# Optimization experiments

Measured on AMD Instinct MI355X. Metric: run time of the kernel, lower is better.

## Reference

```python
import jax, jax.numpy as jnp
import numpy as np

B, T, D, H = 4, 4096, 1024, 64

def setup_inputs() -> dict:
    key = jax.random.key(0)
    k1, k2, k3, k4 = jax.random.split(key, 4)
    scale = 1.0 / np.sqrt(D)
    return {
        "x": jax.random.normal(k1, (B, T, D), dtype=jnp.float32),
        "Wq": jax.random.normal(k2, (D, H), dtype=jnp.float32) * scale,
        "Wk": jax.random.normal(k3, (D, H), dtype=jnp.float32) * scale,
        "Wv": jax.random.normal(k4, (D, H), dtype=jnp.float32) * scale,
    }

def reference(x, Wq, Wk, Wv):
    # Projections (Linear without bias): [B,T,H]
    q = jnp.einsum('btd,dh->bth', x, Wq)
    k = jnp.einsum('btd,dh->bth', x, Wk)
    v = jnp.einsum('btd,dh->bth', x, Wv)
    head_size = q.shape[-1]
    # Full T x T scores, scaled by sqrt(head_size) as in the source
    attn = jnp.einsum('bqh,bkh->bqk', q, k) / jnp.sqrt(jnp.float32(head_size))
    t = x.shape[1]
    causal = jnp.tril(jnp.ones((t, t), dtype=bool))  # [T,T]
    attn = jnp.where(causal[None, :, :], attn, -jnp.inf)
    attn = jax.nn.softmax(attn, axis=-1)
    # dropout prob = 0.0 -> identity
    out = jnp.einsum('bqk,bkh->bqh', attn, v)
    return out
```

## Files before the change

### kernel.cpp

```cpp
#include <hip/hip_runtime.h>
#include <hip/hip_bf16.h>
#include <math.h>

#define BB 4
#define TT 4096
#define DD 1024
#define HH 64
#define MTOT (BB * TT)
#define NCH 4

typedef short short8 __attribute__((ext_vector_type(8)));
typedef float f32x4  __attribute__((ext_vector_type(4)));
typedef unsigned int u32;

__device__ __forceinline__ unsigned short f2bf(float f) {
    unsigned u = __builtin_bit_cast(unsigned, f);
    unsigned r = (u + 0x7fffu + ((u >> 16) & 1u)) >> 16;
    return (unsigned short)r;
}

__device__ __forceinline__ unsigned long long pack4(float a, float b, float c, float d) {
    return (unsigned long long)f2bf(a) |
           ((unsigned long long)f2bf(b) << 16) |
           ((unsigned long long)f2bf(c) << 32) |
           ((unsigned long long)f2bf(d) << 48);
}

__device__ __forceinline__ short8 pack8(float4 a, float4 b) {
    short8 r;
    r[0] = (short)f2bf(a.x); r[1] = (short)f2bf(a.y);
    r[2] = (short)f2bf(a.z); r[3] = (short)f2bf(a.w);
    r[4] = (short)f2bf(b.x); r[5] = (short)f2bf(b.y);
    r[6] = (short)f2bf(b.z); r[7] = (short)f2bf(b.w);
    return r;
}

__device__ __forceinline__ void gl16(const void* g, void* l) {
    __builtin_amdgcn_global_load_lds(
        (const __attribute__((address_space(1))) u32*)g,
        (__attribute__((address_space(3))) u32*)l, 16, 0, 0);
}

#define QOFF  0
#define KOFF  (MTOT * HH)
#define VOFF  (2 * MTOT * HH)
#define BF_TOTAL (3 * MTOT * HH)

__global__ __launch_bounds__(256) void transpose_w(
    const float* __restrict__ Wq, const float* __restrict__ Wk,
    const float* __restrict__ Wv, unsigned short* __restrict__ Wt)
{
    const int w = blockIdx.y;
    const float* W = (w == 0) ? Wq : (w == 1) ? Wk : Wv;
    unsigned short* o = Wt + (size_t)w * 64 * 1024;
    const int t  = threadIdx.x;
    const int n4 = t & 15;
    const int k0 = blockIdx.x * 64 + (t >> 4) * 4;

    float v[4][4];
#pragma unroll
    for (int ii = 0; ii < 4; ++ii) {
        float4 r = *(const float4*)&W[(size_t)(k0 + ii) * HH + n4 * 4];
        v[ii][0] = r.x; v[ii][1] = r.y; v[ii][2] = r.z; v[ii][3] = r.w;
    }
#pragma unroll
    for (int cc = 0; cc < 4; ++cc) {
        unsigned long long pk = pack4(v[0][cc], v[1][cc], v[2][cc], v[3][cc]);
        *(unsigned long long*)&o[(size_t)(n4 * 4 + cc) * 1024 + k0] = pk;
    }
}

__global__ __launch_bounds__(256, 2) void qkv_proj(
    const float* __restrict__ x,
    const unsigned short* __restrict__ Wt,
    unsigned short* __restrict__ qkv)
{
    const int tid   = threadIdx.x;
    const int lane  = tid & 63;
    const int wave  = tid >> 6;
    const int l15   = lane & 15;
    const int quad  = lane >> 4;
    const int m0    = blockIdx.x * 32;
    const int strip = wave & 1;
    const int half  = wave >> 1;

    __shared__ float          Af[2][32 * 64];
    __shared__ unsigned short Bs[2][192 * 64];

    const int ar  = lane >> 4;
    const int as  = lane & 15;
    const int bc  = lane >> 3;
    const int bs2 = (lane & 7) ^ bc;

#define STAGEW(it, p)                                                        \
    {                                                                        \
        const int kc_ = (it) * 64;                                           \
        _Pragma("unroll")                                                    \
        for (int jj = 0; jj < 2; ++jj) {                                     \
            int j   = wave * 2 + jj;                                         \
            int row = 4 * j + ar;                                            \
            int sw  = as ^ (row & 15);                                       \
            gl16(x + (size_t)(m0 + row) * DD + kc_ + sw * 4,                 \
                 &Af[p][j * 256]);                                           \
        }                                                                    \
        _Pragma("unroll")                                                    \
        for (int jj = 0; jj < 6; ++jj) {                                     \
            int j    = wave * 6 + jj;                                        \
            int gcol = 8 * j + bc;                                           \
            gl16(Wt + (size_t)gcol * 1024 + kc_ + bs2 * 8,                   \
                 &Bs[p][j * 512]);                                           \
        }                                                                    \
    }

    f32x4 acc[6];
#pragma unroll
    for (int i = 0; i < 6; ++i) acc[i] = (f32x4){0.f, 0.f, 0.f, 0.f};

    STAGEW(0, 0)
    __syncthreads();
    int p = 0;

    for (int it = 0; it < 16; ++it) {
        if (it < 15) STAGEW(it + 1, p ^ 1)

        const int row = strip * 16 + l15;
#pragma unroll
        for (int ks = 0; ks < 2; ++ks) {
            int c0 = ks * 8 + quad * 2;
            float4 a0 = *(const float4*)&Af[p][row * 64 + ((c0)     ^ l15) * 4];
            float4 a1 = *(const float4*)&Af[p][row * 64 + ((c0 + 1) ^ l15) * 4];
            short8 af = pack8(a0, a1);
            int cb = (ks * 4 + quad) ^ (l15 & 7);
#pragma unroll
            for (int jj = 0; jj < 6; ++jj) {
                int col = (half * 6 + jj) * 16 + l15;
                short8 bfr = *(const short8*)&Bs[p][col * 64 + cb * 8];
                acc[jj] = __builtin_amdgcn_mfma_f32_16x16x32_bf16(af, bfr, acc[jj], 0, 0, 0);
            }
        }
        __syncthreads();
        p ^= 1;
    }
#undef STAGEW

    const float QS = 0.125f * 1.44269504088896f;
    unsigned short* q_bf  = qkv + QOFF;
    unsigned short* k_bf  = qkv + KOFF;
    unsigned short* vt_bf = qkv + VOFF;
#pragma unroll
    for (int jj = 0; jj < 6; ++jj) {
        int g = half * 6 + jj, w = g >> 2, col = (g & 3) * 16 + l15;
#pragma unroll
        for (int r = 0; r < 4; ++r) {
            int m = m0 + strip * 16 + quad * 4 + r;
            float val = acc[jj][r];
            if (w == 0) val *= QS;
            unsigned short bv = f2bf(val);
            if (w == 0)      q_bf[(size_t)m * HH + col] = bv;
            else if (w == 1) k_bf[(size_t)m * HH + col] = bv;
            else {
                int b = m >> 12, t = m & 4095;
                vt_bf[(size_t)b * HH * TT + (size_t)col * TT + t] = bv;
            }
        }
    }
}

__global__ __launch_bounds__(256) void flash_attn(
    const unsigned short* __restrict__ qkv,
    float* __restrict__ Opart,
    float* __restrict__ Mpart,
    float* __restrict__ Lpart)
{
    const int qt = 63 - blockIdx.x;
    const int b  = blockIdx.y;
    const int c  = blockIdx.z;
    if (c * 16 > qt) return;
    const int j0   = c * 16;
    const int jmax = min(j0 + 16, qt + 1);

    const int tid  = threadIdx.x;
    const int lane = tid & 63;
    const int wave = tid >> 6;
    const int l15  = lane & 15;
    const int quad = lane >> 4;

    const unsigned short* q_g  = qkv + QOFF + (size_t)b * TT * HH;
    const unsigned short* k_g  = qkv + KOFF + (size_t)b * TT * HH;
    const unsigned short* vt_g = qkv + VOFF + (size_t)b * HH * TT;

    __shared__ unsigned short Ks[2][128 * 64];
    __shared__ unsigned short Vs[2][64 * 128];
    __shared__ unsigned short Ps[4][16 * 72];
    unsigned short* Pw = &Ps[wave][0];

    const int kr3 = lane >> 3;
    const int kch = lane & 7;
    const int vr2 = lane >> 4;
    const int vch = lane & 15;

#define STAGE(jr_, p_)                                                        \
    {                                                                         \
        const unsigned short* kp = k_g  + (size_t)(jr_) * 64 * HH;            \
        const unsigned short* vp = vt_g + (size_t)(jr_) * 64;                 \
        _Pragma("unroll")                                                     \
        for (int i = 0; i < 4; ++i) {                                         \
            int g = wave * 4 + i;                                             \
            gl16(kp + (size_t)(g * 8 + kr3) * HH + (kch ^ kr3) * 8,           \
                 &Ks[p_][g * 512]);                                           \
        }                                                                     \
        _Pragma("unroll")                                                     \
        for (int i = 0; i < 4; ++i) {                                         \
            int g = wave * 4 + i;                                             \
            int h = g * 4 + vr2;                                              \
            gl16(vp + (size_t)h * TT + (vch ^ (h & 15)) * 8,                  \
                 &Vs[p_][g * 512]);                                           \
        }                                                                     \
    }

    short8 qf[2];
#pragma unroll
    for (int kk = 0; kk < 2; ++kk)
        qf[kk] = *(const short8*)&q_g[(size_t)(qt * 64 + wave * 16 + l15) * HH + kk * 32 + quad * 8];

    f32x4 ov[4];
#pragma unroll
    for (int i = 0; i < 4; ++i) ov[i] = (f32x4){0.f, 0.f, 0.f, 0.f};
    float m_run = -1e30f, l_run = 0.f;

    STAGE(j0, 0)
    __syncthreads();
    int p = 0;

    for (int jr = j0; jr < jmax; jr += 2) {
        const bool two = (jmax - jr) >= 2;

        if (jr + 2 < jmax) STAGE(jr + 2, p ^ 1)

        f32x4 st0[4], st1[4];
#pragma unroll
        for (int i = 0; i < 4; ++i) {
            st0[i] = (f32x4){0.f, 0.f, 0.f, 0.f};
            st1[i] = (f32x4){0.f, 0.f, 0.f, 0.f};
        }
#pragma unroll
        for (int kk = 0; kk < 2; ++kk)
#pragma unroll
            for (int mt = 0; mt < 4; ++mt) {
                short8 a = *(const short8*)&Ks[p][(mt * 16 + l15) * 64 +
                                                  (((kk * 4 + quad) ^ (l15 & 7)) * 8)];
                st0[mt] = __builtin_amdgcn_mfma_f32_16x16x32_bf16(a, qf[kk], st0[mt], 0, 0, 0);
            }
        if (two) {
#pragma unroll
            for (int kk = 0; kk < 2; ++kk)
#pragma unroll
                for (int mt = 0; mt < 4; ++mt) {
                    short8 a = *(const short8*)&Ks[p][(64 + mt * 16 + l15) * 64 +
                                                      (((kk * 4 + quad) ^ (l15 & 7)) * 8)];
                    st1[mt] = __builtin_amdgcn_mfma_f32_16x16x32_bf16(a, qf[kk], st1[mt], 0, 0, 0);
                }
        }

        const int qg = wave * 16 + l15;
        if (jr == qt) {
#pragma unroll
            for (int mt = 0; mt < 4; ++mt)
#pragma unroll
                for (int r = 0; r < 4; ++r)
                    if (mt * 16 + quad * 4 + r > qg) st0[mt][r] = -1e30f;
        } else if (two && jr + 1 == qt) {
#pragma unroll
            for (int mt = 0; mt < 4; ++mt)
#pragma unroll
                for (int r = 0; r < 4; ++r)
                    if (mt * 16 + quad * 4 + r > qg) st1[mt][r] = -1e30f;
        }

        float mloc = -1e30f;
#pragma unroll
        for (int mt = 0; mt < 4; ++mt)
#pragma unroll
            for (int r = 0; r < 4; ++r) mloc = fmaxf(mloc, st0[mt][r]);
        if (two) {
#pragma unroll
            for (int mt = 0; mt < 4; ++mt)
#pragma unroll
                for (int r = 0; r < 4; ++r) mloc = fmaxf(mloc, st1[mt][r]);
        }
        mloc = fmaxf(mloc, __shfl_xor(mloc, 16));
        mloc = fmaxf(mloc, __shfl_xor(mloc, 32));
        const float m_new = fmaxf(m_run, mloc);
        const float alpha = exp2f(m_run - m_new);
        m_run = m_new;

        float ssum = 0.f;
#pragma unroll
        for (int mt = 0; mt < 4; ++mt)
#pragma unroll
            for (int r = 0; r < 4; ++r) {
                float pv = exp2f(st0[mt][r] - m_new);
                st0[mt][r] = pv; ssum += pv;
            }
        if (two) {
#pragma unroll
            for (int mt = 0; mt < 4; ++mt)
#pragma unroll
                for (int r = 0; r < 4; ++r) {
                    float pv = exp2f(st1[mt][r] - m_new);
                    st1[mt][r] = pv; ssum += pv;
                }
        }
        ssum += __shfl_xor(ssum, 16);
        ssum += __shfl_xor(ssum, 32);
        l_run = l_run * alpha + ssum;

        {
            float a0 = __shfl(alpha, quad * 4 + 0);
            float a1 = __shfl(alpha, quad * 4 + 1);
            float a2 = __shfl(alpha, quad * 4 + 2);
            float a3 = __shfl(alpha, quad * 4 + 3);
#pragma unroll
            for (int ht = 0; ht < 4; ++ht) {
                ov[ht][0] *= a0; ov[ht][1] *= a1;
                ov[ht][2] *= a2; ov[ht][3] *= a3;
            }
        }

#pragma unroll
        for (int mt = 0; mt < 4; ++mt) {
            u32 p0, p1;
            asm("v_cvt_pk_bf16_f32 %0, %1, %2" : "=v"(p0) : "v"(st0[mt][0]), "v"(st0[mt][1]));
            asm("v_cvt_pk_bf16_f32 %0, %1, %2" : "=v"(p1) : "v"(st0[mt][2]), "v"(st0[mt][3]));
            uint2 pr; pr.x = p0; pr.y = p1;
            *(uint2*)&Pw[l15 * 72 + mt * 16 + quad * 4] = pr;
        }
#pragma unroll
        for (int kk = 0; kk < 2; ++kk) {
            short8 a = *(const short8*)&Pw[l15 * 72 + kk * 32 + quad * 8];
#pragma unroll
            for (int ht = 0; ht < 4; ++ht) {
                short8 bf = *(const short8*)&Vs[p][(ht * 16 + l15) * 128 +
                                                   (((kk * 4 + quad) ^ l15) * 8)];
                ov[ht] = __builtin_amdgcn_mfma_f32_16x16x32_bf16(a, bf, ov[ht], 0, 0, 0);
            }
        }

        if (two) {
#pragma unroll
            for (int mt = 0; mt < 4; ++mt) {
                u32 p0, p1;
                asm("v_cvt_pk_bf16_f32 %0, %1, %2" : "=v"(p0) : "v"(st1[mt][0]), "v"(st1[mt][1]));
                asm("v_cvt_pk_bf16_f32 %0, %1, %2" : "=v"(p1) : "v"(st1[mt][2]), "v"(st1[mt][3]));
                uint2 pr; pr.x = p0; pr.y = p1;
                *(uint2*)&Pw[l15 * 72 + mt * 16 + quad * 4] = pr;
            }
#pragma unroll
            for (int kk = 0; kk < 2; ++kk) {
                short8 a = *(const short8*)&Pw[l15 * 72 + kk * 32 + quad * 8];
#pragma unroll
                for (int ht = 0; ht < 4; ++ht) {
                    short8 bf = *(const short8*)&Vs[p][(ht * 16 + l15) * 128 +
                                                       (((8 + kk * 4 + quad) ^ l15) * 8)];
                    ov[ht] = __builtin_amdgcn_mfma_f32_16x16x32_bf16(a, bf, ov[ht], 0, 0, 0);
                }
            }
        }

        __syncthreads();
        p ^= 1;
    }
#undef STAGE

    float* Ob = Opart + ((size_t)((b * 64 + qt) * NCH + c)) * 4096;
#pragma unroll
    for (int ht = 0; ht < 4; ++ht)
#pragma unroll
        for (int r = 0; r < 4; ++r)
            Ob[(size_t)(wave * 16 + quad * 4 + r) * HH + ht * 16 + l15] = ov[ht][r];
    if (quad == 0) {
        size_t mi = (size_t)((b * 64 + qt) * NCH + c) * 64 + wave * 16 + l15;
        Mpart[mi] = m_run;
        Lpart[mi] = l_run;
    }
}

__global__ __launch_bounds__(256) void combine(
    const float* __restrict__ Opart,
    const float* __restrict__ Mpart,
    const float* __restrict__ Lpart,
    float* __restrict__ out)
{
    const int qt = blockIdx.x;
    const int b  = blockIdx.y;
    const int nc = (qt >> 4) + 1;
    const int t  = threadIdx.x;
    const int row = t >> 2;
    const int seg = t & 3;

    const size_t base = (size_t)(b * 64 + qt) * NCH;

    float m_c[NCH], M = -1e30f;
    for (int c = 0; c < nc; ++c) {
        m_c[c] = Mpart[(base + c) * 64 + row];
        M = fmaxf(M, m_c[c]);
    }
    float L = 0.f, w_c[NCH];
    for (int c = 0; c < nc; ++c) {
        w_c[c] = exp2f(m_c[c] - M);
        L += w_c[c] * Lpart[(base + c) * 64 + row];
    }
    float invL = 1.0f / L;

    f32x4 o[4];
#pragma unroll
    for (int i = 0; i < 4; ++i) o[i] = (f32x4){0.f, 0.f, 0.f, 0.f};
    for (int c = 0; c < nc; ++c) {
        const float* Ob = Opart + (base + c) * 4096 + (size_t)row * HH + seg * 16;
#pragma unroll
        for (int i = 0; i < 4; ++i) {
            f32x4 v = *(const f32x4*)(Ob + i * 4);
            o[i] += v * w_c[c];
        }
    }
    float* op = out + ((size_t)b * TT + qt * 64 + row) * HH + seg * 16;
#pragma unroll
    for (int i = 0; i < 4; ++i)
        *(f32x4*)(op + i * 4) = o[i] * invL;
}

extern "C" void kernel_launch(void* const* d_in, const int* in_sizes, int n_in,
                              void* d_out, int out_size, void* d_ws, size_t ws_size,
                              hipStream_t stream) {
    const float* x  = (const float*)d_in[0];
    const float* Wq = (const float*)d_in[1];
    const float* Wk = (const float*)d_in[2];
    const float* Wv = (const float*)d_in[3];
    float* out = (float*)d_out;

    unsigned short* qkv = (unsigned short*)d_ws;
    float* Opart = (float*)((char*)d_ws + BF_TOTAL * 2);
    float* Mpart = Opart + (size_t)BB * 64 * NCH * 4096;
    float* Lpart = Mpart + (size_t)BB * 64 * NCH * 64;

    unsigned short* Wt = (unsigned short*)d_out;

    transpose_w<<<dim3(16, 3), 256, 0, stream>>>(Wq, Wk, Wv, Wt);
    qkv_proj<<<dim3(MTOT / 32), 256, 0, stream>>>(x, Wt, qkv);
    flash_attn<<<dim3(64, BB, NCH), 256, 0, stream>>>(qkv, Opart, Mpart, Lpart);
    combine<<<dim3(64, BB), 256, 0, stream>>>(Opart, Mpart, Lpart, out);
}
```

Measured before the change: 163.0 us.

## Keep P in registers, single-buffer V with re-swizzled layout, raise occupancy

Softmax probabilities are packed to bf16 in registers and fed straight to the PV MFMA, removing the per-wave LDS round trip through Ps. V is now single-buffered and loaded inside the same iteration, with a new swizzle and split 8-byte reads that line up with the register layout of P. An extra barrier is added before the PV step. Launch bounds ask for 3 blocks per CU, using the LDS freed by dropping Ps and one V buffer. The cost is that V loads are no longer prefetched an iteration ahead, so their latency sits on the critical path, and the extra barrier adds a sync point.

Measured after the change: 154.9 us. 1.05x faster.

```diff
diff --git a/kernel.cpp b/kernel.cpp
--- a/kernel.cpp
+++ b/kernel.cpp
@@ -12,6 +12,7 @@
 typedef short short8 __attribute__((ext_vector_type(8)));
 typedef float f32x4  __attribute__((ext_vector_type(4)));
 typedef unsigned int u32;
+typedef unsigned long long u64;
 
 __device__ __forceinline__ unsigned short f2bf(float f) {
     unsigned u = __builtin_bit_cast(unsigned, f);
@@ -166,7 +167,7 @@
     }
 }
 
-__global__ __launch_bounds__(256) void flash_attn(
+__global__ __launch_bounds__(256, 3) void flash_attn(
     const unsigned short* __restrict__ qkv,
     float* __restrict__ Opart,
     float* __restrict__ Mpart,
@@ -190,31 +191,32 @@
     const unsigned short* vt_g = qkv + VOFF + (size_t)b * HH * TT;
 
     __shared__ unsigned short Ks[2][128 * 64];
-    __shared__ unsigned short Vs[2][64 * 128];
-    __shared__ unsigned short Ps[4][16 * 72];
-    unsigned short* Pw = &Ps[wave][0];
+    __shared__ unsigned short Vs[64 * 128];
 
     const int kr3 = lane >> 3;
     const int kch = lane & 7;
     const int vr2 = lane >> 4;
     const int vch = lane & 15;
 
-#define STAGE(jr_, p_)                                                        \
+#define STAGE_K(jr_, p_)                                                      \
     {                                                                         \
-        const unsigned short* kp = k_g  + (size_t)(jr_) * 64 * HH;            \
-        const unsigned short* vp = vt_g + (size_t)(jr_) * 64;                 \
+        const unsigned short* kp = k_g + (size_t)(jr_) * 64 * HH;             \
         _Pragma("unroll")                                                     \
         for (int i = 0; i < 4; ++i) {                                         \
             int g = wave * 4 + i;                                             \
             gl16(kp + (size_t)(g * 8 + kr3) * HH + (kch ^ kr3) * 8,           \
                  &Ks[p_][g * 512]);                                           \
         }                                                                     \
+    }
+#define STAGE_V(jr_)                                                          \
+    {                                                                         \
+        const unsigned short* vp = vt_g + (size_t)(jr_) * 64;                 \
         _Pragma("unroll")                                                     \
         for (int i = 0; i < 4; ++i) {                                         \
             int g = wave * 4 + i;                                             \
             int h = g * 4 + vr2;                                              \
-            gl16(vp + (size_t)h * TT + (vch ^ (h & 15)) * 8,                  \
-                 &Vs[p_][g * 512]);                                           \
+            gl16(vp + (size_t)h * TT + (vch ^ ((h >> 1) & 7)) * 8,            \
+                 &Vs[g * 512]);                                               \
         }                                                                     \
     }
 
@@ -228,14 +230,17 @@
     for (int i = 0; i < 4; ++i) ov[i] = (f32x4){0.f, 0.f, 0.f, 0.f};
     float m_run = -1e30f, l_run = 0.f;
 
-    STAGE(j0, 0)
+    STAGE_K(j0, 0)
     __syncthreads();
     int p = 0;
 
+    const int swv = 2 * ((l15 >> 1) & 7);
+
     for (int jr = j0; jr < jmax; jr += 2) {
         const bool two = (jmax - jr) >= 2;
 
-        if (jr + 2 < jmax) STAGE(jr + 2, p ^ 1)
+        STAGE_V(jr)
+        if (jr + 2 < jmax) STAGE_K(jr + 2, p ^ 1)
 
         f32x4 st0[4], st1[4];
 #pragma unroll
@@ -315,6 +320,32 @@
         ssum += __shfl_xor(ssum, 32);
         l_run = l_run * alpha + ssum;
 
+        short8 pa00, pa01, pa10, pa11;
+        {
+            u32* pp = (u32*)&pa00;
+            asm("v_cvt_pk_bf16_f32 %0, %1, %2" : "=v"(pp[0]) : "v"(st0[0][0]), "v"(st0[0][1]));
+            asm("v_cvt_pk_bf16_f32 %0, %1, %2" : "=v"(pp[1]) : "v"(st0[0][2]), "v"(st0[0][3]));
+            asm("v_cvt_pk_bf16_f32 %0, %1, %2" : "=v"(pp[2]) : "v"(st0[1][0]), "v"(st0[1][1]));
+            asm("v_cvt_pk_bf16_f32 %0, %1, %2" : "=v"(pp[3]) : "v"(st0[1][2]), "v"(st0[1][3]));
+            pp = (u32*)&pa01;
+            asm("v_cvt_pk_bf16_f32 %0, %1, %2" : "=v"(pp[0]) : "v"(st0[2][0]), "v"(st0[2][1]));
+            asm("v_cvt_pk_bf16_f32 %0, %1, %2" : "=v"(pp[1]) : "v"(st0[2][2]), "v"(st0[2][3]));
+            asm("v_cvt_pk_bf16_f32 %0, %1, %2" : "=v"(pp[2]) : "v"(st0[3][0]), "v"(st0[3][1]));
+            asm("v_cvt_pk_bf16_f32 %0, %1, %2" : "=v"(pp[3]) : "v"(st0[3][2]), "v"(st0[3][3]));
+        }
+        if (two) {
+            u32* pp = (u32*)&pa10;
+            asm("v_cvt_pk_bf16_f32 %0, %1, %2" : "=v"(pp[0]) : "v"(st1[0][0]), "v"(st1[0][1]));
+            asm("v_cvt_pk_bf16_f32 %0, %1, %2" : "=v"(pp[1]) : "v"(st1[0][2]), "v"(st1[0][3]));
+            asm("v_cvt_pk_bf16_f32 %0, %1, %2" : "=v"(pp[2]) : "v"(st1[1][0]), "v"(st1[1][1]));
+            asm("v_cvt_pk_bf16_f32 %0, %1, %2" : "=v"(pp[3]) : "v"(st1[1][2]), "v"(st1[1][3]));
+            pp = (u32*)&pa11;
+            asm("v_cvt_pk_bf16_f32 %0, %1, %2" : "=v"(pp[0]) : "v"(st1[2][0]), "v"(st1[2][1]));
+            asm("v_cvt_pk_bf16_f32 %0, %1, %2" : "=v"(pp[1]) : "v"(st1[2][2]), "v"(st1[2][3]));
+            asm("v_cvt_pk_bf16_f32 %0, %1, %2" : "=v"(pp[2]) : "v"(st1[3][0]), "v"(st1[3][1]));
+            asm("v_cvt_pk_bf16_f32 %0, %1, %2" : "=v"(pp[3]) : "v"(st1[3][2]), "v"(st1[3][3]));
+        }
+
         {
             float a0 = __shfl(alpha, quad * 4 + 0);
             float a1 = __shfl(alpha, quad * 4 + 1);
@@ -327,42 +358,37 @@
             }
         }
 
-#pragma unroll
-        for (int mt = 0; mt < 4; ++mt) {
-            u32 p0, p1;
-            asm("v_cvt_pk_bf16_f32 %0, %1, %2" : "=v"(p0) : "v"(st0[mt][0]), "v"(st0[mt][1]));
-            asm("v_cvt_pk_bf16_f32 %0, %1, %2" : "=v"(p1) : "v"(st0[mt][2]), "v"(st0[mt][3]));
-            uint2 pr; pr.x = p0; pr.y = p1;
-            *(uint2*)&Pw[l15 * 72 + mt * 16 + quad * 4] = pr;
-        }
+        __syncthreads();
+
 #pragma unroll
         for (int kk = 0; kk < 2; ++kk) {
-            short8 a = *(const short8*)&Pw[l15 * 72 + kk * 32 + quad * 8];
+            short8 a = kk ? pa01 : pa00;
+            int c8 = kk * 8 + quad;
 #pragma unroll
             for (int ht = 0; ht < 4; ++ht) {
-                short8 bf = *(const short8*)&Vs[p][(ht * 16 + l15) * 128 +
-                                                   (((kk * 4 + quad) ^ l15) * 8)];
-                ov[ht] = __builtin_amdgcn_mfma_f32_16x16x32_bf16(a, bf, ov[ht], 0, 0, 0);
-            }
-        }
-
+                int rb = (ht * 16 + l15) * 128;
+                u64 lo = *(const u64*)&Vs[rb + ((c8 ^ swv) << 2)];
+                u64 hi = *(const u64*)&Vs[rb + ((c8 ^ 4 ^ swv) << 2)];
+                short8 vb;
+                ((u64*)&vb)[0] = lo;
+                ((u64*)&vb)[1] = hi;
+                ov[ht] = __builtin_amdgcn_mfma_f32_16x16x32_bf16(a, vb, ov[ht], 0, 0, 0);
+            }
+        }
         if (two) {
 #pragma unroll
-            for (int mt = 0; mt < 4; ++mt) {
-                u32 p0, p1;
-                asm("v_cvt_pk_bf16_f32 %0, %1, %2" : "=v"(p0) : "v"(st1[mt][0]), "v"(st1[mt][1]));
-                asm("v_cvt_pk_bf16_f32 %0, %1, %2" : "=v"(p1) : "v"(st1[mt][2]), "v"(st1[mt][3]));
-                uint2 pr; pr.x = p0; pr.y = p1;
-                *(uint2*)&Pw[l15 * 72 + mt * 16 + quad * 4] = pr;
-            }
-#pragma unroll
             for (int kk = 0; kk < 2; ++kk) {
-                short8 a = *(const short8*)&Pw[l15 * 72 + kk * 32 + quad * 8];
+                short8 a = kk ? pa11 : pa10;
+                int c8 = 16 + kk * 8 + quad;
 #pragma unroll
                 for (int ht = 0; ht < 4; ++ht) {
-                    short8 bf = *(const short8*)&Vs[p][(ht * 16 + l15) * 128 +
-                                                       (((8 + kk * 4 + quad) ^ l15) * 8)];
-                    ov[ht] = __builtin_amdgcn_mfma_f32_16x16x32_bf16(a, bf, ov[ht], 0, 0, 0);
+                    int rb = (ht * 16 + l15) * 128;
+                    u64 lo = *(const u64*)&Vs[rb + ((c8 ^ swv) << 2)];
+                    u64 hi = *(const u64*)&Vs[rb + ((c8 ^ 4 ^ swv) << 2)];
+                    short8 vb;
+                    ((u64*)&vb)[0] = lo;
+                    ((u64*)&vb)[1] = hi;
+                    ov[ht] = __builtin_amdgcn_mfma_f32_16x16x32_bf16(a, vb, ov[ht], 0, 0, 0);
                 }
             }
         }
@@ -370,7 +396,8 @@
         __syncthreads();
         p ^= 1;
     }
-#undef STAGE
+#undef STAGE_K
+#undef STAGE_V
 
     float* Ob = Opart + ((size_t)((b * 64 + qt) * NCH + c)) * 4096;
 #pragma unroll
```

## Process paired query tiles per block sharing K/V tiles, with finer KV chunking

Applied to the files above, without the earlier changes.

Each flash-attention block now handles two adjacent query tiles, so each K/V tile staged into shared memory is reused by both. KV work is split into 8 chunks of 8 tiles instead of 4 of 16, and blocks are mapped through a flattened 1D grid. P is kept in registers instead of going through shared memory, and V reads use a new swizzle. The rescale is skipped when the max does not change, s_setprio wraps the MFMA sections, and the bf16 packing in the projection kernel uses v_cvt_pk_bf16_f32. The change aims to cut LDS traffic per query and improve load balance, at the cost of more registers per thread (launch bounds 256,2) and more partial results for the combine step.

Result: slower. 181.8 us (+11.5%).

```diff
diff --git a/kernel.cpp b/kernel.cpp
--- a/kernel.cpp
+++ b/kernel.cpp
@@ -7,11 +7,12 @@
 #define DD 1024
 #define HH 64
 #define MTOT (BB * TT)
-#define NCH 4
+#define NCH 8
 
 typedef short short8 __attribute__((ext_vector_type(8)));
 typedef float f32x4  __attribute__((ext_vector_type(4)));
 typedef unsigned int u32;
+typedef unsigned long long u64;
 
 __device__ __forceinline__ unsigned short f2bf(float f) {
     unsigned u = __builtin_bit_cast(unsigned, f);
@@ -24,15 +25,6 @@
            ((unsigned long long)f2bf(b) << 16) |
            ((unsigned long long)f2bf(c) << 32) |
            ((unsigned long long)f2bf(d) << 48);
-}
-
-__device__ __forceinline__ short8 pack8(float4 a, float4 b) {
-    short8 r;
-    r[0] = (short)f2bf(a.x); r[1] = (short)f2bf(a.y);
-    r[2] = (short)f2bf(a.z); r[3] = (short)f2bf(a.w);
-    r[4] = (short)f2bf(b.x); r[5] = (short)f2bf(b.y);
-    r[6] = (short)f2bf(b.z); r[7] = (short)f2bf(b.w);
-    return r;
 }
 
 __device__ __forceinline__ void gl16(const void* g, void* l) {
@@ -129,7 +121,14 @@
             int c0 = ks * 8 + quad * 2;
             float4 a0 = *(const float4*)&Af[p][row * 64 + ((c0)     ^ l15) * 4];
             float4 a1 = *(const float4*)&Af[p][row * 64 + ((c0 + 1) ^ l15) * 4];
-            short8 af = pack8(a0, a1);
+            short8 af;
+            {
+                u32* ap = (u32*)&af;
+                asm("v_cvt_pk_bf16_f32 %0, %1, %2" : "=v"(ap[0]) : "v"(a0.x), "v"(a0.y));
+                asm("v_cvt_pk_bf16_f32 %0, %1, %2" : "=v"(ap[1]) : "v"(a0.z), "v"(a0.w));
+                asm("v_cvt_pk_bf16_f32 %0, %1, %2" : "=v"(ap[2]) : "v"(a1.x), "v"(a1.y));
+                asm("v_cvt_pk_bf16_f32 %0, %1, %2" : "=v"(ap[3]) : "v"(a1.z), "v"(a1.w));
+            }
             int cb = (ks * 4 + quad) ^ (l15 & 7);
 #pragma unroll
             for (int jj = 0; jj < 6; ++jj) {
@@ -166,18 +165,22 @@
     }
 }
 
-__global__ __launch_bounds__(256) void flash_attn(
+__global__ __launch_bounds__(256, 2) void flash_attn(
     const unsigned short* __restrict__ qkv,
     float* __restrict__ Opart,
     float* __restrict__ Mpart,
     float* __restrict__ Lpart)
 {
-    const int qt = 63 - blockIdx.x;
-    const int b  = blockIdx.y;
-    const int c  = blockIdx.z;
-    if (c * 16 > qt) return;
-    const int j0   = c * 16;
-    const int jmax = min(j0 + 16, qt + 1);
+    const int gid = blockIdx.x;
+    const int b   = gid & 3;
+    const int u   = gid >> 2;
+    const int c   = u & 7;
+    const int pr  = u >> 3;
+    const int qtB = 63 - 2 * pr;
+    const int qtA = qtB - 1;
+    if (c * 8 > qtB) return;
+    const int j0   = c * 8;
+    const int jmax = min(j0 + 8, qtB + 1);
 
     const int tid  = threadIdx.x;
     const int lane = tid & 63;
@@ -189,199 +192,222 @@
     const unsigned short* k_g  = qkv + KOFF + (size_t)b * TT * HH;
     const unsigned short* vt_g = qkv + VOFF + (size_t)b * HH * TT;
 
-    __shared__ unsigned short Ks[2][128 * 64];
-    __shared__ unsigned short Vs[2][64 * 128];
-    __shared__ unsigned short Ps[4][16 * 72];
-    unsigned short* Pw = &Ps[wave][0];
-
-    const int kr3 = lane >> 3;
-    const int kch = lane & 7;
-    const int vr2 = lane >> 4;
-    const int vch = lane & 15;
-
-#define STAGE(jr_, p_)                                                        \
+    __shared__ unsigned short Ks[2][64 * 64];
+    __shared__ unsigned short Vs[2][64 * 64];
+
+    const int lr8 = lane >> 3;
+    const int lc8 = lane & 7;
+
+#define STAGE(j_, p_)                                                         \
     {                                                                         \
-        const unsigned short* kp = k_g  + (size_t)(jr_) * 64 * HH;            \
-        const unsigned short* vp = vt_g + (size_t)(jr_) * 64;                 \
+        const unsigned short* kp = k_g + (size_t)(j_) * 64 * HH;              \
+        const unsigned short* vp = vt_g + (size_t)(j_) * 64;                  \
         _Pragma("unroll")                                                     \
-        for (int i = 0; i < 4; ++i) {                                         \
-            int g = wave * 4 + i;                                             \
-            gl16(kp + (size_t)(g * 8 + kr3) * HH + (kch ^ kr3) * 8,           \
+        for (int i = 0; i < 2; ++i) {                                         \
+            int g = wave * 2 + i;                                             \
+            gl16(kp + (size_t)(g * 8 + lr8) * HH + ((lc8 ^ lr8) << 3),        \
                  &Ks[p_][g * 512]);                                           \
         }                                                                     \
         _Pragma("unroll")                                                     \
-        for (int i = 0; i < 4; ++i) {                                         \
-            int g = wave * 4 + i;                                             \
-            int h = g * 4 + vr2;                                              \
-            gl16(vp + (size_t)h * TT + (vch ^ (h & 15)) * 8,                  \
+        for (int i = 0; i < 2; ++i) {                                         \
+            int g = wave * 2 + i;                                             \
+            int sw = ((g & 1) << 2) | (lr8 >> 1);                             \
+            gl16(vp + (size_t)(g * 8 + lr8) * TT + ((lc8 ^ sw) << 3),         \
                  &Vs[p_][g * 512]);                                           \
         }                                                                     \
     }
 
-    short8 qf[2];
-#pragma unroll
-    for (int kk = 0; kk < 2; ++kk)
-        qf[kk] = *(const short8*)&q_g[(size_t)(qt * 64 + wave * 16 + l15) * HH + kk * 32 + quad * 8];
-
-    f32x4 ov[4];
-#pragma unroll
-    for (int i = 0; i < 4; ++i) ov[i] = (f32x4){0.f, 0.f, 0.f, 0.f};
-    float m_run = -1e30f, l_run = 0.f;
+    short8 qfA[2], qfB[2];
+#pragma unroll
+    for (int kk = 0; kk < 2; ++kk) {
+        qfA[kk] = *(const short8*)&q_g[(size_t)(qtA * 64 + wave * 16 + l15) * HH + kk * 32 + quad * 8];
+        qfB[kk] = *(const short8*)&q_g[(size_t)(qtB * 64 + wave * 16 + l15) * HH + kk * 32 + quad * 8];
+    }
+
+    f32x4 ovA[4], ovB[4];
+#pragma unroll
+    for (int i = 0; i < 4; ++i) {
+        ovA[i] = (f32x4){0.f, 0.f, 0.f, 0.f};
+        ovB[i] = (f32x4){0.f, 0.f, 0.f, 0.f};
+    }
+    float mA = -1e30f, lA = 0.f, mB = -1e30f, lB = 0.f;
 
     STAGE(j0, 0)
     __syncthreads();
     int p = 0;
 
-    for (int jr = j0; jr < jmax; jr += 2) {
-        const bool two = (jmax - jr) >= 2;
-
-        if (jr + 2 < jmax) STAGE(jr + 2, p ^ 1)
-
-        f32x4 st0[4], st1[4];
+    const int qg  = wave * 16 + l15;
+    const int swv = (l15 >> 1) & 7;
+
+    for (int j = j0; j < jmax; ++j) {
+        if (j + 1 < jmax) STAGE(j + 1, p ^ 1)
+        const bool doA = (j <= qtA);
+
+        f32x4 sA[4], sB[4];
 #pragma unroll
         for (int i = 0; i < 4; ++i) {
-            st0[i] = (f32x4){0.f, 0.f, 0.f, 0.f};
-            st1[i] = (f32x4){0.f, 0.f, 0.f, 0.f};
-        }
+            sA[i] = (f32x4){0.f, 0.f, 0.f, 0.f};
+            sB[i] = (f32x4){0.f, 0.f, 0.f, 0.f};
+        }
+        __builtin_amdgcn_s_setprio(1);
 #pragma unroll
         for (int kk = 0; kk < 2; ++kk)
 #pragma unroll
             for (int mt = 0; mt < 4; ++mt) {
                 short8 a = *(const short8*)&Ks[p][(mt * 16 + l15) * 64 +
-                                                  (((kk * 4 + quad) ^ (l15 & 7)) * 8)];
-                st0[mt] = __builtin_amdgcn_mfma_f32_16x16x32_bf16(a, qf[kk], st0[mt], 0, 0, 0);
-            }
-        if (two) {
-#pragma unroll
-            for (int kk = 0; kk < 2; ++kk)
-#pragma unroll
-                for (int mt = 0; mt < 4; ++mt) {
-                    short8 a = *(const short8*)&Ks[p][(64 + mt * 16 + l15) * 64 +
-                                                      (((kk * 4 + quad) ^ (l15 & 7)) * 8)];
-                    st1[mt] = __builtin_amdgcn_mfma_f32_16x16x32_bf16(a, qf[kk], st1[mt], 0, 0, 0);
+                                                  (((kk * 4 + quad) ^ (l15 & 7)) << 3)];
+                if (doA) sA[mt] = __builtin_amdgcn_mfma_f32_16x16x32_bf16(a, qfA[kk], sA[mt], 0, 0, 0);
+                sB[mt] = __builtin_amdgcn_mfma_f32_16x16x32_bf16(a, qfB[kk], sB[mt], 0, 0, 0);
+            }
+        __builtin_amdgcn_s_setprio(0);
+
+        short8 paA0 = {0}, paA1 = {0}, paB0 = {0}, paB1 = {0};
+        if (doA) {
+            if (j == qtA) {
+#pragma unroll
+                for (int mt = 0; mt < 4; ++mt)
+#pragma unroll
+                    for (int r = 0; r < 4; ++r)
+                        if (mt * 16 + quad * 4 + r > qg) sA[mt][r] = -1e30f;
+            }
+            float ml = -1e30f;
+#pragma unroll
+            for (int mt = 0; mt < 4; ++mt)
+#pragma unroll
+                for (int r = 0; r < 4; ++r) ml = fmaxf(ml, sA[mt][r]);
+            ml = fmaxf(ml, __shfl_xor(ml, 16));
+            ml = fmaxf(ml, __shfl_xor(ml, 32));
+            if (!__all(ml <= mA)) {
+                float mn = fmaxf(mA, ml);
+                float al = exp2f(mA - mn);
+                mA = mn;
+                lA *= al;
+                float a0 = __shfl(al, quad * 4 + 0);
+                float a1 = __shfl(al, quad * 4 + 1);
+                float a2 = __shfl(al, quad * 4 + 2);
+                float a3 = __shfl(al, quad * 4 + 3);
+#pragma unroll
+                for (int ht = 0; ht < 4; ++ht) {
+                    ovA[ht][0] *= a0; ovA[ht][1] *= a1;
+                    ovA[ht][2] *= a2; ovA[ht][3] *= a3;
                 }
-        }
-
-        const int qg = wave * 16 + l15;
-        if (jr == qt) {
+            }
+            float ss = 0.f;
 #pragma unroll
             for (int mt = 0; mt < 4; ++mt)
 #pragma unroll
-                for (int r = 0; r < 4; ++r)
-                    if (mt * 16 + quad * 4 + r > qg) st0[mt][r] = -1e30f;
-        } else if (two && jr + 1 == qt) {
+                for (int r = 0; r < 4; ++r) {
+                    float pv = exp2f(sA[mt][r] - mA);
+                    sA[mt][r] = pv; ss += pv;
+                }
+            ss += __shfl_xor(ss, 16);
+            ss += __shfl_xor(ss, 32);
+            lA += ss;
+            u32* pp = (u32*)&paA0;
+            asm("v_cvt_pk_bf16_f32 %0, %1, %2" : "=v"(pp[0]) : "v"(sA[0][0]), "v"(sA[0][1]));
+            asm("v_cvt_pk_bf16_f32 %0, %1, %2" : "=v"(pp[1]) : "v"(sA[0][2]), "v"(sA[0][3]));
+            asm("v_cvt_pk_bf16_f32 %0, %1, %2" : "=v"(pp[2]) : "v"(sA[1][0]), "v"(sA[1][1]));
+            asm("v_cvt_pk_bf16_f32 %0, %1, %2" : "=v"(pp[3]) : "v"(sA[1][2]), "v"(sA[1][3]));
+            pp = (u32*)&paA1;
+            asm("v_cvt_pk_bf16_f32 %0, %1, %2" : "=v"(pp[0]) : "v"(sA[2][0]), "v"(sA[2][1]));
+            asm("v_cvt_pk_bf16_f32 %0, %1, %2" : "=v"(pp[1]) : "v"(sA[2][2]), "v"(sA[2][3]));
+            asm("v_cvt_pk_bf16_f32 %0, %1, %2" : "=v"(pp[2]) : "v"(sA[3][0]), "v"(sA[3][1]));
+            asm("v_cvt_pk_bf16_f32 %0, %1, %2" : "=v"(pp[3]) : "v"(sA[3][2]), "v"(sA[3][3]));
+        }
+
+        {
+            if (j == qtB) {
+#pragma unroll
+                for (int mt = 0; mt < 4; ++mt)
+#pragma unroll
+                    for (int r = 0; r < 4; ++r)
+                        if (mt * 16 + quad * 4 + r > qg) sB[mt][r] = -1e30f;
+            }
+            float ml = -1e30f;
 #pragma unroll
             for (int mt = 0; mt < 4; ++mt)
 #pragma unroll
-                for (int r = 0; r < 4; ++r)
-                    if (mt * 16 + quad * 4 + r > qg) st1[mt][r] = -1e30f;
-        }
-
-        float mloc = -1e30f;
-#pragma unroll
-        for (int mt = 0; mt < 4; ++mt)
-#pragma unroll
-            for (int r = 0; r < 4; ++r) mloc = fmaxf(mloc, st0[mt][r]);
-        if (two) {
+                for (int r = 0; r < 4; ++r) ml = fmaxf(ml, sB[mt][r]);
+            ml = fmaxf(ml, __shfl_xor(ml, 16));
+            ml = fmaxf(ml, __shfl_xor(ml, 32));
+            if (!__all(ml <= mB)) {
+                float mn = fmaxf(mB, ml);
+                float al = exp2f(mB - mn);
+                mB = mn;
+                lB *= al;
+                float a0 = __shfl(al, quad * 4 + 0);
+                float a1 = __shfl(al, quad * 4 + 1);
+                float a2 = __shfl(al, quad * 4 + 2);
+                float a3 = __shfl(al, quad * 4 + 3);
+#pragma unroll
+                for (int ht = 0; ht < 4; ++ht) {
+                    ovB[ht][0] *= a0; ovB[ht][1] *= a1;
+                    ovB[ht][2] *= a2; ovB[ht][3] *= a3;
+                }
+            }
+            float ss = 0.f;
 #pragma unroll
             for (int mt = 0; mt < 4; ++mt)
 #pragma unroll
-                for (int r = 0; r < 4; ++r) mloc = fmaxf(mloc, st1[mt][r]);
-        }
-        mloc = fmaxf(mloc, __shfl_xor(mloc, 16));
-        mloc = fmaxf(mloc, __shfl_xor(mloc, 32));
-        const float m_new = fmaxf(m_run, mloc);
-        const float alpha = exp2f(m_run - m_new);
-        m_run = m_new;
-
-        float ssum = 0.f;
-#pragma unroll
-        for (int mt = 0; mt < 4; ++mt)
-#pragma unroll
-            for (int r = 0; r < 4; ++r) {
-                float pv = exp2f(st0[mt][r] - m_new);
-                st0[mt][r] = pv; ssum += pv;
-            }
-        if (two) {
-#pragma unroll
-            for (int mt = 0; mt < 4; ++mt)
-#pragma unroll
                 for (int r = 0; r < 4; ++r) {
-                    float pv = exp2f(st1[mt][r] - m_new);
-                    st1[mt][r] = pv; ssum += pv;
+                    float pv = exp2f(sB[mt][r] - mB);
+                    sB[mt][r] = pv; ss += pv;
                 }
-        }
-        ssum += __shfl_xor(ssum, 16);
-        ssum += __shfl_xor(ssum, 32);
-        l_run = l_run * alpha + ssum;
-
-        {
-            float a0 = __shfl(alpha, quad * 4 + 0);
-            float a1 = __shfl(alpha, quad * 4 + 1);
-            float a2 = __shfl(alpha, quad * 4 + 2);
-            float a3 = __shfl(alpha, quad * 4 + 3);
+            ss += __shfl_xor(ss, 16);
+            ss += __shfl_xor(ss, 32);
+            lB += ss;
+            u32* pp = (u32*)&paB0;
+            asm("v_cvt_pk_bf16_f32 %0, %1, %2" : "=v"(pp[0]) : "v"(sB[0][0]), "v"(sB[0][1]));
+            asm("v_cvt_pk_bf16_f32 %0, %1, %2" : "=v"(pp[1]) : "v"(sB[0][2]), "v"(sB[0][3]));
+            asm("v_cvt_pk_bf16_f32 %0, %1, %2" : "=v"(pp[2]) : "v"(sB[1][0]), "v"(sB[1][1]));
+            asm("v_cvt_pk_bf16_f32 %0, %1, %2" : "=v"(pp[3]) : "v"(sB[1][2]), "v"(sB[1][3]));
+            pp = (u32*)&paB1;
+            asm("v_cvt_pk_bf16_f32 %0, %1, %2" : "=v"(pp[0]) : "v"(sB[2][0]), "v"(sB[2][1]));
+            asm("v_cvt_pk_bf16_f32 %0, %1, %2" : "=v"(pp[1]) : "v"(sB[2][2]), "v"(sB[2][3]));
+            asm("v_cvt_pk_bf16_f32 %0, %1, %2" : "=v"(pp[2]) : "v"(sB[3][0]), "v"(sB[3][1]));
+            asm("v_cvt_pk_bf16_f32 %0, %1, %2" : "=v"(pp[3]) : "v"(sB[3][2]), "v"(sB[3][3]));
+        }
+
+        __builtin_amdgcn_s_setprio(1);
+#pragma unroll
+        for (int kk = 0; kk < 2; ++kk) {
+            short8 aA = kk ? paA1 : paA0;
+            short8 aB = kk ? paB1 : paB0;
+            int cl = kk * 4 + (quad >> 1);
+            int sub = (quad & 1) << 2;
 #pragma unroll
             for (int ht = 0; ht < 4; ++ht) {
-                ov[ht][0] *= a0; ov[ht][1] *= a1;
-                ov[ht][2] *= a2; ov[ht][3] *= a3;
-            }
-        }
-
-#pragma unroll
-        for (int mt = 0; mt < 4; ++mt) {
-            u32 p0, p1;
-            asm("v_cvt_pk_bf16_f32 %0, %1, %2" : "=v"(p0) : "v"(st0[mt][0]), "v"(st0[mt][1]));
-            asm("v_cvt_pk_bf16_f32 %0, %1, %2" : "=v"(p1) : "v"(st0[mt][2]), "v"(st0[mt][3]));
-            uint2 pr; pr.x = p0; pr.y = p1;
-            *(uint2*)&Pw[l15 * 72 + mt * 16 + quad * 4] = pr;
-        }
-#pragma unroll
-        for (int kk = 0; kk < 2; ++kk) {
-            short8 a = *(const short8*)&Pw[l15 * 72 + kk * 32 + quad * 8];
-#pragma unroll
-            for (int ht = 0; ht < 4; ++ht) {
-                short8 bf = *(const short8*)&Vs[p][(ht * 16 + l15) * 128 +
-                                                   (((kk * 4 + quad) ^ l15) * 8)];
-                ov[ht] = __builtin_amdgcn_mfma_f32_16x16x32_bf16(a, bf, ov[ht], 0, 0, 0);
-            }
-        }
-
-        if (two) {
-#pragma unroll
-            for (int mt = 0; mt < 4; ++mt) {
-                u32 p0, p1;
-                asm("v_cvt_pk_bf16_f32 %0, %1, %2" : "=v"(p0) : "v"(st1[mt][0]), "v"(st1[mt][1]));
-                asm("v_cvt_pk_bf16_f32 %0, %1, %2" : "=v"(p1) : "v"(st1[mt][2]), "v"(st1[mt][3]));
-                uint2 pr; pr.x = p0; pr.y = p1;
-                *(uint2*)&Pw[l15 * 72 + mt * 16 + quad * 4] = pr;
-            }
-#pragma unroll
-            for (int kk = 0; kk < 2; ++kk) {
-                short8 a = *(const short8*)&Pw[l15 * 72 + kk * 32 + quad * 8];
-#pragma unroll
-                for (int ht = 0; ht < 4; ++ht) {
-                    short8 bf = *(const short8*)&Vs[p][(ht * 16 + l15) * 128 +
-                                                       (((8 + kk * 4 + quad) ^ l15) * 8)];
-                    ov[ht] = __builtin_amdgcn_mfma_f32_16x16x32_bf16(a, bf, ov[ht], 0, 0, 0);
-                }
-            }
-        }
+                int rb = (ht * 16 + l15) * 64;
+                u64 lo = *(const u64*)&Vs[p][rb + (((cl)     ^ swv) << 3) + sub];
+                u64 hi = *(const u64*)&Vs[p][rb + (((cl ^ 2) ^ swv) << 3) + sub];
+                short8 vb;
+                ((u64*)&vb)[0] = lo;
+                ((u64*)&vb)[1] = hi;
+                if (doA) ovA[ht] = __builtin_amdgcn_mfma_f32_16x16x32_bf16(aA, vb, ovA[ht], 0, 0, 0);
+                ovB[ht] = __builtin_amdgcn_mfma_f32_16x16x32_bf16(aB, vb, ovB[ht], 0, 0, 0);
+            }
+        }
+        __builtin_amdgcn_s_setprio(0);
 
         __syncthreads();
         p ^= 1;
     }
 #undef STAGE
 
-    float* Ob = Opart + ((size_t)((b * 64 + qt) * NCH + c)) * 4096;
+    float* ObA = Opart + ((size_t)((b * 64 + qtA) * NCH + c)) * 4096;
+    float* ObB = Opart + ((size_t)((b * 64 + qtB) * NCH + c)) * 4096;
 #pragma unroll
     for (int ht = 0; ht < 4; ++ht)
 #pragma unroll
-        for (int r = 0; r < 4; ++r)
-            Ob[(size_t)(wave * 16 + quad * 4 + r) * HH + ht * 16 + l15] = ov[ht][r];
+        for (int r = 0; r < 4; ++r) {
+            ObA[(size_t)(wave * 16 + quad * 4 + r) * HH + ht * 16 + l15] = ovA[ht][r];
+            ObB[(size_t)(wave * 16 + quad * 4 + r) * HH + ht * 16 + l15] = ovB[ht][r];
+        }
     if (quad == 0) {
-        size_t mi = (size_t)((b * 64 + qt) * NCH + c) * 64 + wave * 16 + l15;
-        Mpart[mi] = m_run;
-        Lpart[mi] = l_run;
+        size_t miA = (size_t)((b * 64 + qtA) * NCH + c) * 64 + wave * 16 + l15;
+        size_t miB = (size_t)((b * 64 + qtB) * NCH + c) * 64 + wave * 16 + l15;
+        Mpart[miA] = mA; Lpart[miA] = lA;
+        Mpart[miB] = mB; Lpart[miB] = lB;
     }
 }
 
@@ -393,36 +419,32 @@
 {
     const int qt = blockIdx.x;
     const int b  = blockIdx.y;
-    const int nc = (qt >> 4) + 1;
+    const int nc = (qt >> 3) + 1;
     const int t  = threadIdx.x;
     const int row = t >> 2;
     const int seg = t & 3;
 
     const size_t base = (size_t)(b * 64 + qt) * NCH;
 
-    float m_c[NCH], M = -1e30f;
-    for (int c = 0; c < nc; ++c) {
-        m_c[c] = Mpart[(base + c) * 64 + row];
-        M = fmaxf(M, m_c[c]);
-    }
-    float L = 0.f, w_c[NCH];
-    for (int c = 0; c < nc; ++c) {
-        w_c[c] = exp2f(m_c[c] - M);
-        L += w_c[c] * Lpart[(base + c) * 64 + row];
-    }
-    float invL = 1.0f / L;
-
+    float M = -1e30f;
+    for (int c = 0; c < nc; ++c)
+        M = fmaxf(M, Mpart[(base + c) * 64 + row]);
+
+    float L = 0.f;
     f32x4 o[4];
 #pragma unroll
     for (int i = 0; i < 4; ++i) o[i] = (f32x4){0.f, 0.f, 0.f, 0.f};
     for (int c = 0; c < nc; ++c) {
+        float w = exp2f(Mpart[(base + c) * 64 + row] - M);
+        L += w * Lpart[(base + c) * 64 + row];
         const float* Ob = Opart + (base + c) * 4096 + (size_t)row * HH + seg * 16;
 #pragma unroll
         for (int i = 0; i < 4; ++i) {
             f32x4 v = *(const f32x4*)(Ob + i * 4);
-            o[i] += v * w_c[c];
-        }
-    }
+            o[i] += v * w;
+        }
+    }
+    float invL = 1.0f / L;
     float* op = out + ((size_t)b * TT + qt * 64 + row) * HH + seg * 16;
 #pragma unroll
     for (int i = 0; i < 4; ++i)
@@ -447,6 +469,6 @@
 
     transpose_w<<<dim3(16, 3), 256, 0, stream>>>(Wq, Wk, Wv, Wt);
     qkv_proj<<<dim3(MTOT / 32), 256, 0, stream>>>(x, Wt, qkv);
-    flash_attn<<<dim3(64, BB, NCH), 256, 0, stream>>>(qkv, Opart, Mpart, Lpart);
+    flash_attn<<<dim3(1024), 256, 0, stream>>>(qkv, Opart, Mpart, Lpart);
     combine<<<dim3(64, BB), 256, 0, stream>>>(Opart, Mpart, Lpart, out);
 }
```
